# Performance work log

Measured on AMD Instinct MI355X. Metric: run time of the kernel, lower is better.

## Reference

```python
import jax, jax.numpy as jnp
import numpy as np

N_NODES = 50000
N_EDGES = 800000
N_ATOMS = 100
HID = 128
N_LAYERS = 3
OUT_LAYERS = 2
OUT_DIM = 1
N_GRAPHS = 1024
EPS = 1e-12  # F.normalize eps


def setup_inputs() -> dict:
    key = jax.random.key(0)
    ks = jax.random.split(key, 12)
    s = 0.05
    x_ori = jax.random.randint(ks[0], (N_NODES,), 0, N_ATOMS)
    edge_index = jax.random.randint(ks[1], (2, N_EDGES), 0, N_NODES)
    edge_attr = jax.random.normal(ks[2], (N_EDGES, 1), jnp.float32)
    batch_ids = jnp.sort(jax.random.randint(ks[3], (N_NODES,), 0, N_GRAPHS))
    embd_w = jax.random.normal(ks[4], (N_ATOMS, HID), jnp.float32) * s
    gamma_w = jnp.ones((N_LAYERS, N_ATOMS, 1), jnp.float32)  # reset_parameters sets ones
    w_atom_W = jax.random.normal(ks[5], (N_LAYERS, HID, HID), jnp.float32) * s
    w_atom_b = jax.random.normal(ks[6], (N_LAYERS, HID), jnp.float32) * s
    lin_W = jax.random.normal(ks[7], (OUT_LAYERS, HID, HID), jnp.float32) * s
    lin_b = jax.random.normal(ks[8], (OUT_LAYERS, HID), jnp.float32) * s
    wp_W = jax.random.normal(ks[9], (HID, OUT_DIM), jnp.float32) * s
    wp_b = jax.random.normal(ks[10], (OUT_DIM,), jnp.float32) * s
    return dict(x_ori=x_ori, edge_index=edge_index, edge_attr=edge_attr,
                batch_ids=batch_ids, embd_w=embd_w, gamma_w=gamma_w,
                w_atom_W=w_atom_W, w_atom_b=w_atom_b, lin_W=lin_W, lin_b=lin_b,
                wp_W=wp_W, wp_b=wp_b)


def reference(x_ori, edge_index, edge_attr, batch_ids, embd_w, gamma_w,
              w_atom_W, w_atom_b, lin_W, lin_b, wp_W, wp_b):
    src, dst = edge_index[0], edge_index[1]
    x = embd_w[x_ori]  # [N, H]
    for l in range(N_LAYERS):
        h = jax.nn.relu(x @ w_atom_W[l] + w_atom_b[l])            # [N, H]
        gam = jax.nn.sigmoid(gamma_w[l])[x_ori][dst]              # [E, 1]
        ew = jnp.exp(-gam * edge_attr ** 2)                       # [E, 1]
        msg = ew * h[src]                                         # [E, H] gather+weight
        agg = jax.ops.segment_sum(msg, dst, num_segments=N_NODES) # scatter-add
        y = agg + x
        nrm = jnp.maximum(jnp.linalg.norm(y, axis=1, keepdims=True), EPS)
        x = y / nrm                                               # F.normalize(., 2, 1)
    for i in range(OUT_LAYERS):
        x = jax.nn.relu(x @ lin_W[i] + lin_b[i])
    m_x = jax.ops.segment_sum(x, batch_ids, num_segments=N_GRAPHS)  # [G, H]
    props = m_x @ wp_W + wp_b                                      # [G, 1]
    return jnp.squeeze(props, axis=1)                              # [G]
```

## Files before the change

kernel.cpp:

```cpp
#include <hip/hip_runtime.h>
#include <hip/hip_bf16.h>
#include <math.h>

typedef __hip_bfloat16 bf16;
typedef unsigned int uint;
typedef unsigned short ushort;
typedef __attribute__((ext_vector_type(8))) short short8;
typedef __attribute__((ext_vector_type(4))) float f32x4;

#define HID 128
#define NN 50000
#define NE 800000
#define NG 1024
#define NA 100
#define CAP 64

__device__ __forceinline__ uint bf16_rne_hi(float f) {
    uint u = __float_as_uint(f);
    return (u + 0x7fffu + ((u >> 16) & 1u)) & 0xffff0000u;
}
__device__ __forceinline__ uint pack_bf16x2(float lo, float hi) {
    return (bf16_rne_hi(lo) >> 16) | bf16_rne_hi(hi);
}
__device__ __forceinline__ ushort bf16_rne(float f) {
    uint u = __float_as_uint(f);
    return (ushort)((u + 0x7fffu + ((u >> 16) & 1u)) >> 16);
}
__device__ __forceinline__ float load_f(const void* p, int i, int f32) {
    return f32 ? ((const float*)p)[i]
               : __uint_as_float((uint)((const ushort*)p)[i] << 16);
}
__device__ __forceinline__ int detect_f32(const void* emb) {
    const ushort* p = (const ushort*)emb;
    int lane = threadIdx.x & 63;
    float v = __uint_as_float((uint)p[lane * 4] << 16);
    int bad0 = (!(v == v) || fabsf(v) > 1e4f || (v != 0.0f && fabsf(v) < 1e-10f));
    float w = __uint_as_float((uint)p[lane * 4 + 2] << 16);
    int bad1 = (!(w == w) || fabsf(w) > 1e4f || (w != 0.0f && fabsf(w) < 1e-10f));
    int cnt = __popcll(__ballot(bad0)) + __popcll(__ballot(bad1));
    return cnt > 16;
}

#define EMB_BLKS   ((NN * 64) / 256)
#define PACKW_BLKS (5 * 16384 / 256)
#define CVT_CNT    (300 + 384 + 256 + 128 + 1)
#define CVT_BLKS   5
#define INITC_BLKS ((NN + 255) / 256)
#define PREP_B1    EMB_BLKS
#define PREP_B2    (PREP_B1 + PACKW_BLKS)
#define PREP_B3    (PREP_B2 + CVT_BLKS)
#define PREP_B4    (PREP_B3 + INITC_BLKS)
#define PREP_B5    (PREP_B4 + 4)
#define PREP_GRID  (PREP_B5 + 1)

__global__ void prep_k(const int* __restrict__ xo, const void* __restrict__ emb,
                       const void* __restrict__ gamw, const void* __restrict__ wAW,
                       const void* __restrict__ wAb, const void* __restrict__ linW,
                       const void* __restrict__ linb, const void* __restrict__ wpW,
                       const void* __restrict__ wpb,
                       uint* __restrict__ xb, ushort* __restrict__ Wp,
                       float* __restrict__ f_sgam, float* __restrict__ f_wAb,
                       float* __restrict__ f_linb, float* __restrict__ f_wp,
                       float* __restrict__ f_wpb, int* __restrict__ cursor,
                       float* __restrict__ grf, int* __restrict__ flag) {
    int f32 = detect_f32(emb);
    int b = blockIdx.x, t = threadIdx.x;
    if (b < PREP_B1) {
        int g = b * 256 + t;
        int node = g >> 6, c2 = g & 63;
        int base = xo[node] * HID + c2 * 2;
        xb[g] = pack_bf16x2(load_f(emb, base, f32), load_f(emb, base + 1, f32));
    } else if (b < PREP_B2) {
        int t2 = (b - PREP_B1) * 256 + t;
        int i   = t2 & 7;
        int n   = (t2 >> 3) & 15;
        int q   = (t2 >> 7) & 3;
        int j16 = (t2 >> 9) & 7;
        int ks  = (t2 >> 12) & 3;
        int mat = t2 >> 14;
        int k = ks * 32 + q * 8 + i;
        int j = j16 * 16 + n;
        const void* W = (mat < 3) ? wAW : linW;
        int off = ((mat < 3) ? mat : (mat - 3)) * 16384 + k * HID + j;
        Wp[t2] = bf16_rne(load_f(W, off, f32));
    } else if (b < PREP_B3) {
        int idx = (b - PREP_B2) * 256 + t;
        if (idx < 300) {
            float v = load_f(gamw, idx, f32);
            f_sgam[idx] = 1.0f / (1.0f + __expf(-v));
        } else if (idx < 684) {
            f_wAb[idx - 300] = load_f(wAb, idx - 300, f32);
        } else if (idx < 940) {
            f_linb[idx - 684] = load_f(linb, idx - 684, f32);
        } else if (idx < 1068) {
            f_wp[idx - 940] = load_f(wpW, idx - 940, f32);
        } else if (idx < CVT_CNT) {
            f_wpb[0] = load_f(wpb, 0, f32);
        }
    } else if (b < PREP_B4) {
        int n = (b - PREP_B3) * 256 + t;
        if (n < NN) cursor[n] = n * CAP;
    } else if (b < PREP_B5) {
        grf[(b - PREP_B4) * 256 + t] = 0.0f;
    } else {
        if (t == 0) *flag = f32;
    }
}

__device__ __forceinline__ void gemm_core(const uint* __restrict__ xb,
                                          const ushort* __restrict__ Wp,
                                          const float* __restrict__ bias,
                                          int m0, int lane,
                                          f32x4 acc0[8], f32x4 acc1[8]) {
    int ln15 = lane & 15;
    int q    = lane >> 4;
    int mA = min(m0 + ln15, NN - 1);
    int mB = min(m0 + 16 + ln15, NN - 1);
    const short8* A8 = (const short8*)xb;
    const short8* B8 = (const short8*)Wp;
#pragma unroll
    for (int j16 = 0; j16 < 8; ++j16) {
        float bv = bias[j16 * 16 + ln15];
        acc0[j16] = (f32x4){bv, bv, bv, bv};
        acc1[j16] = acc0[j16];
    }
#pragma unroll
    for (int ks = 0; ks < 4; ++ks) {
        short8 a0 = A8[mA * 16 + ks * 4 + q];
        short8 a1 = A8[mB * 16 + ks * 4 + q];
#pragma unroll
        for (int j16 = 0; j16 < 8; ++j16) {
            short8 b = B8[(ks * 8 + j16) * 64 + q * 16 + ln15];
            acc0[j16] = __builtin_amdgcn_mfma_f32_16x16x32_bf16(a0, b, acc0[j16], 0, 0, 0);
            acc1[j16] = __builtin_amdgcn_mfma_f32_16x16x32_bf16(a1, b, acc1[j16], 0, 0, 0);
        }
    }
}

__device__ __forceinline__ void gemm_store(f32x4 acc0[8], f32x4 acc1[8],
                                           int m0, int lane, uint* __restrict__ outb) {
    int ln15 = lane & 15;
    int q    = lane >> 4;
    ushort* ob = (ushort*)outb;
#pragma unroll
    for (int reg = 0; reg < 4; ++reg) {
        int n0 = m0 + q * 4 + reg;
        int n1 = n0 + 16;
#pragma unroll
        for (int j16 = 0; j16 < 8; ++j16) {
            if (n0 < NN)
                ob[(size_t)n0 * HID + j16 * 16 + ln15] = bf16_rne(fmaxf(acc0[j16][reg], 0.0f));
            if (n1 < NN)
                ob[(size_t)n1 * HID + j16 * 16 + ln15] = bf16_rne(fmaxf(acc1[j16][reg], 0.0f));
        }
    }
}

#define GEMM_BLKS ((NN + 127) / 128)
#define SCAT_BLKS (NE / 4 / 256)
__global__ __launch_bounds__(256) void work2_k(const uint* __restrict__ xb,
                                               const ushort* __restrict__ Wp,
                                               const float* __restrict__ bias,
                                               uint* __restrict__ outb,
                                               const int* __restrict__ esrc,
                                               const int* __restrict__ edst,
                                               const void* __restrict__ ea,
                                               const void* __restrict__ emb,
                                               int* __restrict__ cursor,
                                               uint* __restrict__ csr) {
    int b = blockIdx.x;
    if (b < GEMM_BLKS) {
        f32x4 acc0[8], acc1[8];
        int m0 = b * 128 + (threadIdx.x >> 6) * 32;
        gemm_core(xb, Wp, bias, m0, threadIdx.x & 63, acc0, acc1);
        gemm_store(acc0, acc1, m0, threadIdx.x & 63, outb);
    } else {
        int f32 = detect_f32(emb);
        int e0 = ((b - GEMM_BLKS) * 256 + threadIdx.x) * 4;
        int4 s4 = *(const int4*)(esrc + e0);
        int4 d4 = *(const int4*)(edst + e0);
        float a0, a1, a2, a3;
        if (f32) {
            float4 f = *(const float4*)((const float*)ea + e0);
            a0 = f.x; a1 = f.y; a2 = f.z; a3 = f.w;
        } else {
            ushort4 u = *(const ushort4*)((const ushort*)ea + e0);
            a0 = __uint_as_float((uint)u.x << 16);
            a1 = __uint_as_float((uint)u.y << 16);
            a2 = __uint_as_float((uint)u.z << 16);
            a3 = __uint_as_float((uint)u.w << 16);
        }
        int p0 = atomicAdd(&cursor[d4.x], 1);
        int p1 = atomicAdd(&cursor[d4.y], 1);
        int p2 = atomicAdd(&cursor[d4.z], 1);
        int p3 = atomicAdd(&cursor[d4.w], 1);
        if (p0 < d4.x * CAP + CAP) csr[p0] = (uint)(s4.x & 0xffff) | bf16_rne_hi(a0 * a0);
        if (p1 < d4.y * CAP + CAP) csr[p1] = (uint)(s4.y & 0xffff) | bf16_rne_hi(a1 * a1);
        if (p2 < d4.z * CAP + CAP) csr[p2] = (uint)(s4.z & 0xffff) | bf16_rne_hi(a2 * a2);
        if (p3 < d4.w * CAP + CAP) csr[p3] = (uint)(s4.w & 0xffff) | bf16_rne_hi(a3 * a3);
    }
}

__global__ __launch_bounds__(512) void gg_k(const int* __restrict__ cursor,
                                            const uint* __restrict__ csr,
                                            const int* __restrict__ xo,
                                            const float* __restrict__ sgam,
                                            const uint* __restrict__ hb_in,
                                            uint* __restrict__ xb,
                                            const ushort* __restrict__ Wp,
                                            const float* __restrict__ bias,
                                            uint* __restrict__ hb_out) {
    __shared__ uint lds_a[2048];
    int t = threadIdx.x;
    int w = t >> 6, lane = t & 63;
    int n0 = blockIdx.x * 32;

#pragma unroll
    for (int j4 = 0; j4 < 4; ++j4) {
        int j = w * 4 + j4;
        int n = n0 + j;
        if (n < NN) {
            int deg = min(cursor[n] - n * CAP, CAP);
            const uint* cp = csr + n * CAP;
            float g = sgam[xo[n]];
            float ax = 0.0f, ay = 0.0f;
            for (int e = 0; e < deg; e += 8) {
                uint4 c0 = *(const uint4*)(cp + e);
                uint4 c1 = *(const uint4*)(cp + e + 4);
                uint cc[8];
                cc[0] = c0.x; cc[1] = c0.y; cc[2] = c0.z; cc[3] = c0.w;
                cc[4] = c1.x; cc[5] = c1.y; cc[6] = c1.z; cc[7] = c1.w;
#pragma unroll
                for (int i = 1; i < 8; ++i) cc[i] = (e + i < deg) ? cc[i] : cc[0];
                uint v[8];
#pragma unroll
                for (int i = 0; i < 8; ++i) v[i] = hb_in[(cc[i] & 0xffffu) * 64 + lane];
                float we[8];
#pragma unroll
                for (int i = 0; i < 8; ++i) {
                    float x = __expf(-g * __uint_as_float(cc[i] & 0xffff0000u));
                    we[i] = (e + i < deg) ? x : 0.0f;
                }
#pragma unroll
                for (int i = 0; i < 8; ++i) {
                    ax = fmaf(we[i], __uint_as_float(v[i] << 16), ax);
                    ay = fmaf(we[i], __uint_as_float(v[i] & 0xffff0000u), ay);
                }
            }
            uint xv = xb[n * 64 + lane];
            float yx = ax + __uint_as_float(xv << 16);
            float yy = ay + __uint_as_float(xv & 0xffff0000u);
            float ss = yx * yx + yy * yy;
#pragma unroll
            for (int m = 32; m; m >>= 1) ss += __shfl_xor(ss, m);
            float inv = 1.0f / fmaxf(sqrtf(ss), 1e-12f);
            uint o = pack_bf16x2(yx * inv, yy * inv);
            xb[n * 64 + lane] = o;
            int rt = j >> 4, m = j & 15;
            int ks = lane >> 4, q = (lane >> 2) & 3;
            lds_a[(((rt * 4 + ks) * 64) + q * 16 + m) * 4 + (lane & 3)] = o;
        }
    }
    __syncthreads();

    int ln15 = lane & 15, q = lane >> 4;
    const short8* A8 = (const short8*)lds_a;
    const short8* B8 = (const short8*)Wp;
    f32x4 acc[2];
    {
        float bv = bias[w * 16 + ln15];
        acc[0] = (f32x4){bv, bv, bv, bv};
        acc[1] = acc[0];
    }
#pragma unroll
    for (int ks = 0; ks < 4; ++ks) {
        short8 b = B8[(ks * 8 + w) * 64 + q * 16 + ln15];
#pragma unroll
        for (int rt = 0; rt < 2; ++rt) {
            short8 a = A8[(rt * 4 + ks) * 64 + lane];
            acc[rt] = __builtin_amdgcn_mfma_f32_16x16x32_bf16(a, b, acc[rt], 0, 0, 0);
        }
    }
    ushort* ob = (ushort*)hb_out;
#pragma unroll
    for (int rt = 0; rt < 2; ++rt) {
#pragma unroll
        for (int reg = 0; reg < 4; ++reg) {
            int n = n0 + rt * 16 + q * 4 + reg;
            if (n < NN)
                ob[(size_t)n * HID + w * 16 + ln15] = bf16_rne(fmaxf(acc[rt][reg], 0.0f));
        }
    }
}

__global__ __launch_bounds__(256) void gemm5_graph_k(const uint* __restrict__ xb,
                                                     const ushort* __restrict__ Wp,
                                                     const float* __restrict__ bias,
                                                     const float* __restrict__ wp,
                                                     const int* __restrict__ batch,
                                                     float* __restrict__ grf) {
    int lane = threadIdx.x & 63;
    int ln15 = lane & 15;
    int q    = lane >> 4;
    int m0 = blockIdx.x * 128 + (threadIdx.x >> 6) * 32;
    f32x4 acc0[8], acc1[8];
    gemm_core(xb, Wp, bias, m0, lane, acc0, acc1);
    float wpv[8];
#pragma unroll
    for (int j16 = 0; j16 < 8; ++j16) wpv[j16] = wp[j16 * 16 + ln15];
#pragma unroll
    for (int half = 0; half < 2; ++half) {
#pragma unroll
        for (int reg = 0; reg < 4; ++reg) {
            float s = 0.0f;
#pragma unroll
            for (int j16 = 0; j16 < 8; ++j16) {
                float v = half ? acc1[j16][reg] : acc0[j16][reg];
                s = fmaf(fmaxf(v, 0.0f), wpv[j16], s);
            }
#pragma unroll
            for (int m = 1; m < 16; m <<= 1) s += __shfl_xor(s, m);
            int n = m0 + half * 16 + q * 4 + reg;
            if (ln15 == 0 && n < NN) atomicAdd(&grf[batch[n]], s);
        }
    }
}

__global__ void out_k(const float* __restrict__ grf, const float* __restrict__ wpb,
                      void* __restrict__ out, const int* __restrict__ flag) {
    int g = blockIdx.x * 256 + threadIdx.x;
    if (g >= NG) return;
    float r = grf[g] + wpb[0];
    if (*flag) ((float*)out)[g] = r;
    else       ((bf16*)out)[g] = __float2bfloat16(r);
}

extern "C" void kernel_launch(void* const* d_in, const int* in_sizes, int n_in,
                              void* d_out, int out_size, void* d_ws, size_t ws_size,
                              hipStream_t stream) {
    const int*  xo    = (const int*)d_in[0];
    const int*  ei    = (const int*)d_in[1];
    const int*  src   = ei;
    const int*  dst   = ei + NE;
    const void* ea    = d_in[2];
    const int*  batch = (const int*)d_in[3];
    const void* emb   = d_in[4];
    const void* gamw  = d_in[5];
    const void* wAW   = d_in[6];
    const void* wAb   = d_in[7];
    const void* linW  = d_in[8];
    const void* linb  = d_in[9];
    const void* wpW   = d_in[10];
    const void* wpb   = d_in[11];

    uint*  xb     = (uint*)d_ws;
    uint*  hA     = xb + (size_t)NN * 64;
    uint*  hB     = hA + (size_t)NN * 64;
    uint*  csr    = hB + (size_t)NN * 64;
    int*   cursor = (int*)(csr + (size_t)NN * CAP);
    float* grf    = (float*)(cursor + NN);
    float* P      = grf + NG;
    float* f_sgam = P;
    float* f_wAb  = f_sgam + 304;
    float* f_linb = f_wAb + 384;
    float* f_wp   = f_linb + 256;
    float* f_wpb  = f_wp + 128;
    int*   flag   = (int*)(f_wpb + 8);
    ushort* Wp    = (ushort*)(flag + 8);

    prep_k<<<PREP_GRID, 256, 0, stream>>>(xo, emb, gamw, wAW, wAb, linW, linb, wpW, wpb,
                                          xb, Wp, f_sgam, f_wAb, f_linb, f_wp, f_wpb,
                                          cursor, grf, flag);

    work2_k<<<GEMM_BLKS + SCAT_BLKS, 256, 0, stream>>>(xb, Wp, f_wAb, hA,
                                                       src, dst, ea, emb, cursor, csr);

    const int GG_GRID = (NN + 31) / 32;
    gg_k<<<GG_GRID, 512, 0, stream>>>(cursor, csr, xo, f_sgam,       hA, xb,
                                      Wp + 1 * 16384, f_wAb + 128, hB);
    gg_k<<<GG_GRID, 512, 0, stream>>>(cursor, csr, xo, f_sgam + 100, hB, xb,
                                      Wp + 2 * 16384, f_wAb + 256, hA);
    gg_k<<<GG_GRID, 512, 0, stream>>>(cursor, csr, xo, f_sgam + 200, hA, xb,
                                      Wp + 3 * 16384, f_linb,       hB);

    gemm5_graph_k<<<GEMM_BLKS, 256, 0, stream>>>(hB, Wp + 4 * 16384, f_linb + HID,
                                                 f_wp, batch, grf);
    out_k<<<(NG + 255) / 256, 256, 0, stream>>>(grf, f_wpb, d_out, flag);
}
```

Before: 295.5 us.

## Bucket edges by destination before CSR build and fuse final linear into last layer

Edge scattering into per-node CSR slots now happens in two passes. First, edges are binned by destination into 98 buckets of 512 nodes, using block-local histograms and one global atomic per bucket. Then one block per bucket writes the CSR using LDS atomics for degrees, replacing global per-node cursor atomics. The last graph layer kernel is templated to also run the final linear layer and the per-graph readout from LDS, which removes the separate gemm5 kernel and the write and re-read of hB. It adds a memset, and the buckets have a fixed capacity of 10240, so records beyond that are silently dropped if a bucket overflows.

```diff
diff --git a/kernel.cpp b/kernel.cpp
--- a/kernel.cpp
+++ b/kernel.cpp
@@ -14,6 +14,9 @@
 #define NG 1024
 #define NA 100
 #define CAP 64
+
+#define NB   98
+#define RCAP 10240
 
 __device__ __forceinline__ uint bf16_rne_hi(float f) {
     uint u = __float_as_uint(f);
@@ -41,37 +44,94 @@
     return cnt > 16;
 }
 
+#define A_BLKS     196
 #define EMB_BLKS   ((NN * 64) / 256)
 #define PACKW_BLKS (5 * 16384 / 256)
 #define CVT_CNT    (300 + 384 + 256 + 128 + 1)
 #define CVT_BLKS   5
-#define INITC_BLKS ((NN + 255) / 256)
-#define PREP_B1    EMB_BLKS
-#define PREP_B2    (PREP_B1 + PACKW_BLKS)
-#define PREP_B3    (PREP_B2 + CVT_BLKS)
-#define PREP_B4    (PREP_B3 + INITC_BLKS)
-#define PREP_B5    (PREP_B4 + 4)
-#define PREP_GRID  (PREP_B5 + 1)
+#define PR_B1      A_BLKS
+#define PR_B2      (PR_B1 + EMB_BLKS)
+#define PR_B3      (PR_B2 + PACKW_BLKS)
+#define PR_B4      (PR_B3 + CVT_BLKS)
+#define PR_B5      (PR_B4 + 4)
+#define PREP_GRID  (PR_B5 + 1)
 
 __global__ void prep_k(const int* __restrict__ xo, const void* __restrict__ emb,
                        const void* __restrict__ gamw, const void* __restrict__ wAW,
                        const void* __restrict__ wAb, const void* __restrict__ linW,
                        const void* __restrict__ linb, const void* __restrict__ wpW,
                        const void* __restrict__ wpb,
+                       const int* __restrict__ esrc, const int* __restrict__ edst,
+                       const void* __restrict__ ea,
                        uint* __restrict__ xb, ushort* __restrict__ Wp,
                        float* __restrict__ f_sgam, float* __restrict__ f_wAb,
                        float* __restrict__ f_linb, float* __restrict__ f_wp,
-                       float* __restrict__ f_wpb, int* __restrict__ cursor,
+                       float* __restrict__ f_wpb,
+                       uint2* __restrict__ rec, int* __restrict__ bcur,
                        float* __restrict__ grf, int* __restrict__ flag) {
     int f32 = detect_f32(emb);
     int b = blockIdx.x, t = threadIdx.x;
-    if (b < PREP_B1) {
-        int g = b * 256 + t;
+    if (b < PR_B1) {
+        __shared__ int hist[NB];
+        __shared__ int obase[NB];
+        if (t < NB) hist[t] = 0;
+        __syncthreads();
+        int  dv[16];
+        uint rv[16];
+#pragma unroll
+        for (int k = 0; k < 4; ++k) {
+            int e = b * 4096 + k * 1024 + t * 4;
+            if (e + 3 < NE) {
+                int4 s4 = *(const int4*)(esrc + e);
+                int4 d4 = *(const int4*)(edst + e);
+                float a0, a1, a2, a3;
+                if (f32) {
+                    float4 f = *(const float4*)((const float*)ea + e);
+                    a0 = f.x; a1 = f.y; a2 = f.z; a3 = f.w;
+                } else {
+                    ushort4 u = *(const ushort4*)((const ushort*)ea + e);
+                    a0 = __uint_as_float((uint)u.x << 16);
+                    a1 = __uint_as_float((uint)u.y << 16);
+                    a2 = __uint_as_float((uint)u.z << 16);
+                    a3 = __uint_as_float((uint)u.w << 16);
+                }
+                atomicAdd(&hist[d4.x >> 9], 1);
+                atomicAdd(&hist[d4.y >> 9], 1);
+                atomicAdd(&hist[d4.z >> 9], 1);
+                atomicAdd(&hist[d4.w >> 9], 1);
+                dv[k * 4 + 0] = d4.x; rv[k * 4 + 0] = (uint)(s4.x & 0xffff) | ((uint)bf16_rne(a0 * a0) << 16);
+                dv[k * 4 + 1] = d4.y; rv[k * 4 + 1] = (uint)(s4.y & 0xffff) | ((uint)bf16_rne(a1 * a1) << 16);
+                dv[k * 4 + 2] = d4.z; rv[k * 4 + 2] = (uint)(s4.z & 0xffff) | ((uint)bf16_rne(a2 * a2) << 16);
+                dv[k * 4 + 3] = d4.w; rv[k * 4 + 3] = (uint)(s4.w & 0xffff) | ((uint)bf16_rne(a3 * a3) << 16);
+            } else {
+                dv[k * 4 + 0] = dv[k * 4 + 1] = dv[k * 4 + 2] = dv[k * 4 + 3] = -1;
+                rv[k * 4 + 0] = rv[k * 4 + 1] = rv[k * 4 + 2] = rv[k * 4 + 3] = 0;
+            }
+        }
+        __syncthreads();
+        if (t < NB) {
+            int c = hist[t];
+            obase[t] = c ? atomicAdd(&bcur[t], c) : 0;
+            hist[t] = 0;
+        }
+        __syncthreads();
+#pragma unroll
+        for (int k = 0; k < 16; ++k) {
+            int d = dv[k];
+            if (d >= 0) {
+                int bb = d >> 9;
+                int r = atomicAdd(&hist[bb], 1);
+                int idx = obase[bb] + r;
+                if (idx < RCAP) rec[bb * RCAP + idx] = make_uint2(rv[k], (uint)d);
+            }
+        }
+    } else if (b < PR_B2) {
+        int g = (b - PR_B1) * 256 + t;
         int node = g >> 6, c2 = g & 63;
         int base = xo[node] * HID + c2 * 2;
         xb[g] = pack_bf16x2(load_f(emb, base, f32), load_f(emb, base + 1, f32));
-    } else if (b < PREP_B2) {
-        int t2 = (b - PREP_B1) * 256 + t;
+    } else if (b < PR_B3) {
+        int t2 = (b - PR_B2) * 256 + t;
         int i   = t2 & 7;
         int n   = (t2 >> 3) & 15;
         int q   = (t2 >> 7) & 3;
@@ -83,8 +143,8 @@
         const void* W = (mat < 3) ? wAW : linW;
         int off = ((mat < 3) ? mat : (mat - 3)) * 16384 + k * HID + j;
         Wp[t2] = bf16_rne(load_f(W, off, f32));
-    } else if (b < PREP_B3) {
-        int idx = (b - PREP_B2) * 256 + t;
+    } else if (b < PR_B4) {
+        int idx = (b - PR_B3) * 256 + t;
         if (idx < 300) {
             float v = load_f(gamw, idx, f32);
             f_sgam[idx] = 1.0f / (1.0f + __expf(-v));
@@ -97,11 +157,8 @@
         } else if (idx < CVT_CNT) {
             f_wpb[0] = load_f(wpb, 0, f32);
         }
-    } else if (b < PREP_B4) {
-        int n = (b - PREP_B3) * 256 + t;
-        if (n < NN) cursor[n] = n * CAP;
-    } else if (b < PREP_B5) {
-        grf[(b - PREP_B4) * 256 + t] = 0.0f;
+    } else if (b < PR_B5) {
+        grf[(b - PR_B4) * 256 + t] = 0.0f;
     } else {
         if (t == 0) *flag = f32;
     }
@@ -156,52 +213,41 @@
     }
 }
 
-#define GEMM_BLKS ((NN + 127) / 128)
-#define SCAT_BLKS (NE / 4 / 256)
-__global__ __launch_bounds__(256) void work2_k(const uint* __restrict__ xb,
+#define G1_BLKS ((NN + 255) / 256)
+__global__ __launch_bounds__(512) void work2_k(const uint* __restrict__ xb,
                                                const ushort* __restrict__ Wp,
                                                const float* __restrict__ bias,
                                                uint* __restrict__ outb,
-                                               const int* __restrict__ esrc,
-                                               const int* __restrict__ edst,
-                                               const void* __restrict__ ea,
-                                               const void* __restrict__ emb,
-                                               int* __restrict__ cursor,
-                                               uint* __restrict__ csr) {
-    int b = blockIdx.x;
-    if (b < GEMM_BLKS) {
+                                               const uint2* __restrict__ rec,
+                                               const int* __restrict__ bcur,
+                                               uint* __restrict__ csr,
+                                               int* __restrict__ degarr) {
+    int b = blockIdx.x, t = threadIdx.x;
+    if (b < NB) {
+        __shared__ int ldeg[512];
+        ldeg[t] = 0;
+        __syncthreads();
+        int cnt = min(bcur[b], RCAP);
+        int nb0 = b << 9;
+        for (int i = t; i < cnt; i += 512) {
+            uint2 r = rec[b * RCAP + i];
+            int dst = (int)r.y;
+            int p = atomicAdd(&ldeg[dst - nb0], 1);
+            if (p < CAP) csr[dst * CAP + p] = r.x;
+        }
+        __syncthreads();
+        int n = nb0 + t;
+        if (n < NN) degarr[n] = min(ldeg[t], CAP);
+    } else {
         f32x4 acc0[8], acc1[8];
-        int m0 = b * 128 + (threadIdx.x >> 6) * 32;
-        gemm_core(xb, Wp, bias, m0, threadIdx.x & 63, acc0, acc1);
-        gemm_store(acc0, acc1, m0, threadIdx.x & 63, outb);
-    } else {
-        int f32 = detect_f32(emb);
-        int e0 = ((b - GEMM_BLKS) * 256 + threadIdx.x) * 4;
-        int4 s4 = *(const int4*)(esrc + e0);
-        int4 d4 = *(const int4*)(edst + e0);
-        float a0, a1, a2, a3;
-        if (f32) {
-            float4 f = *(const float4*)((const float*)ea + e0);
-            a0 = f.x; a1 = f.y; a2 = f.z; a3 = f.w;
-        } else {
-            ushort4 u = *(const ushort4*)((const ushort*)ea + e0);
-            a0 = __uint_as_float((uint)u.x << 16);
-            a1 = __uint_as_float((uint)u.y << 16);
-            a2 = __uint_as_float((uint)u.z << 16);
-            a3 = __uint_as_float((uint)u.w << 16);
-        }
-        int p0 = atomicAdd(&cursor[d4.x], 1);
-        int p1 = atomicAdd(&cursor[d4.y], 1);
-        int p2 = atomicAdd(&cursor[d4.z], 1);
-        int p3 = atomicAdd(&cursor[d4.w], 1);
-        if (p0 < d4.x * CAP + CAP) csr[p0] = (uint)(s4.x & 0xffff) | bf16_rne_hi(a0 * a0);
-        if (p1 < d4.y * CAP + CAP) csr[p1] = (uint)(s4.y & 0xffff) | bf16_rne_hi(a1 * a1);
-        if (p2 < d4.z * CAP + CAP) csr[p2] = (uint)(s4.z & 0xffff) | bf16_rne_hi(a2 * a2);
-        if (p3 < d4.w * CAP + CAP) csr[p3] = (uint)(s4.w & 0xffff) | bf16_rne_hi(a3 * a3);
-    }
-}
-
-__global__ __launch_bounds__(512) void gg_k(const int* __restrict__ cursor,
+        int m0 = (b - NB) * 256 + (t >> 6) * 32;
+        gemm_core(xb, Wp, bias, m0, t & 63, acc0, acc1);
+        gemm_store(acc0, acc1, m0, t & 63, outb);
+    }
+}
+
+template<int LAST>
+__global__ __launch_bounds__(512) void gg_k(const int* __restrict__ degarr,
                                             const uint* __restrict__ csr,
                                             const int* __restrict__ xo,
                                             const float* __restrict__ sgam,
@@ -209,8 +255,15 @@
                                             uint* __restrict__ xb,
                                             const ushort* __restrict__ Wp,
                                             const float* __restrict__ bias,
-                                            uint* __restrict__ hb_out) {
-    __shared__ uint lds_a[2048];
+                                            uint* __restrict__ hb_out,
+                                            const ushort* __restrict__ Wp2,
+                                            const float* __restrict__ bias2,
+                                            const float* __restrict__ wp,
+                                            const int* __restrict__ batch,
+                                            float* __restrict__ grf) {
+    __shared__ uint  lds_a[2048];
+    __shared__ uint  lds_b[LAST ? 2048 : 1];
+    __shared__ float lds_p[LAST ? 256 : 1];
     int t = threadIdx.x;
     int w = t >> 6, lane = t & 63;
     int n0 = blockIdx.x * 32;
@@ -220,7 +273,7 @@
         int j = w * 4 + j4;
         int n = n0 + j;
         if (n < NN) {
-            int deg = min(cursor[n] - n * CAP, CAP);
+            int deg = degarr[n];
             const uint* cp = csr + n * CAP;
             float g = sgam[xo[n]];
             float ax = 0.0f, ay = 0.0f;
@@ -255,7 +308,7 @@
             for (int m = 32; m; m >>= 1) ss += __shfl_xor(ss, m);
             float inv = 1.0f / fmaxf(sqrtf(ss), 1e-12f);
             uint o = pack_bf16x2(yx * inv, yy * inv);
-            xb[n * 64 + lane] = o;
+            if (!LAST) xb[n * 64 + lane] = o;
             int rt = j >> 4, m = j & 15;
             int ks = lane >> 4, q = (lane >> 2) & 3;
             lds_a[(((rt * 4 + ks) * 64) + q * 16 + m) * 4 + (lane & 3)] = o;
@@ -274,54 +327,73 @@
     }
 #pragma unroll
     for (int ks = 0; ks < 4; ++ks) {
-        short8 b = B8[(ks * 8 + w) * 64 + q * 16 + ln15];
+        short8 b = B8[(ks * 8 + w) * 64 + lane];
 #pragma unroll
         for (int rt = 0; rt < 2; ++rt) {
             short8 a = A8[(rt * 4 + ks) * 64 + lane];
             acc[rt] = __builtin_amdgcn_mfma_f32_16x16x32_bf16(a, b, acc[rt], 0, 0, 0);
         }
     }
-    ushort* ob = (ushort*)hb_out;
-#pragma unroll
-    for (int rt = 0; rt < 2; ++rt) {
-#pragma unroll
-        for (int reg = 0; reg < 4; ++reg) {
-            int n = n0 + rt * 16 + q * 4 + reg;
-            if (n < NN)
-                ob[(size_t)n * HID + w * 16 + ln15] = bf16_rne(fmaxf(acc[rt][reg], 0.0f));
-        }
-    }
-}
-
-__global__ __launch_bounds__(256) void gemm5_graph_k(const uint* __restrict__ xb,
-                                                     const ushort* __restrict__ Wp,
-                                                     const float* __restrict__ bias,
-                                                     const float* __restrict__ wp,
-                                                     const int* __restrict__ batch,
-                                                     float* __restrict__ grf) {
-    int lane = threadIdx.x & 63;
-    int ln15 = lane & 15;
-    int q    = lane >> 4;
-    int m0 = blockIdx.x * 128 + (threadIdx.x >> 6) * 32;
-    f32x4 acc0[8], acc1[8];
-    gemm_core(xb, Wp, bias, m0, lane, acc0, acc1);
-    float wpv[8];
-#pragma unroll
-    for (int j16 = 0; j16 < 8; ++j16) wpv[j16] = wp[j16 * 16 + ln15];
-#pragma unroll
-    for (int half = 0; half < 2; ++half) {
-#pragma unroll
-        for (int reg = 0; reg < 4; ++reg) {
+    if (!LAST) {
+        ushort* ob = (ushort*)hb_out;
+#pragma unroll
+        for (int rt = 0; rt < 2; ++rt) {
+#pragma unroll
+            for (int reg = 0; reg < 4; ++reg) {
+                int n = n0 + rt * 16 + q * 4 + reg;
+                if (n < NN)
+                    ob[(size_t)n * HID + w * 16 + ln15] = bf16_rne(fmaxf(acc[rt][reg], 0.0f));
+            }
+        }
+    } else {
+        ushort* sb = (ushort*)lds_b;
+        int c  = w * 16 + ln15;
+        int c2 = c >> 1, cb = c2 & 3, cq = (c2 >> 2) & 3, cks = c2 >> 4, lohi = c & 1;
+#pragma unroll
+        for (int rt = 0; rt < 2; ++rt) {
+#pragma unroll
+            for (int reg = 0; reg < 4; ++reg) {
+                int m = q * 4 + reg;
+                int uidx = ((rt * 4 + cks) * 64 + cq * 16 + m) * 4 + cb;
+                sb[uidx * 2 + lohi] = bf16_rne(fmaxf(acc[rt][reg], 0.0f));
+            }
+        }
+        __syncthreads();
+        const short8* A8b = (const short8*)lds_b;
+        const short8* B8b = (const short8*)Wp2;
+        f32x4 acc3[2];
+        {
+            float bv = bias2[w * 16 + ln15];
+            acc3[0] = (f32x4){bv, bv, bv, bv};
+            acc3[1] = acc3[0];
+        }
+#pragma unroll
+        for (int ks = 0; ks < 4; ++ks) {
+            short8 bb = B8b[(ks * 8 + w) * 64 + lane];
+#pragma unroll
+            for (int rt = 0; rt < 2; ++rt) {
+                short8 a = A8b[(rt * 4 + ks) * 64 + lane];
+                acc3[rt] = __builtin_amdgcn_mfma_f32_16x16x32_bf16(a, bb, acc3[rt], 0, 0, 0);
+            }
+        }
+        float wv = wp[w * 16 + ln15];
+#pragma unroll
+        for (int rt = 0; rt < 2; ++rt) {
+#pragma unroll
+            for (int reg = 0; reg < 4; ++reg) {
+                float p = fmaxf(acc3[rt][reg], 0.0f) * wv;
+                p += __shfl_xor(p, 1); p += __shfl_xor(p, 2);
+                p += __shfl_xor(p, 4); p += __shfl_xor(p, 8);
+                if (ln15 == 0) lds_p[(rt * 16 + q * 4 + reg) * 8 + w] = p;
+            }
+        }
+        __syncthreads();
+        if (t < 32) {
             float s = 0.0f;
 #pragma unroll
-            for (int j16 = 0; j16 < 8; ++j16) {
-                float v = half ? acc1[j16][reg] : acc0[j16][reg];
-                s = fmaf(fmaxf(v, 0.0f), wpv[j16], s);
-            }
-#pragma unroll
-            for (int m = 1; m < 16; m <<= 1) s += __shfl_xor(s, m);
-            int n = m0 + half * 16 + q * 4 + reg;
-            if (ln15 == 0 && n < NN) atomicAdd(&grf[batch[n]], s);
+            for (int k = 0; k < 8; ++k) s += lds_p[t * 8 + k];
+            int n = n0 + t;
+            if (n < NN) atomicAdd(&grf[batch[n]], s);
         }
     }
 }
@@ -356,9 +428,10 @@
     uint*  xb     = (uint*)d_ws;
     uint*  hA     = xb + (size_t)NN * 64;
     uint*  hB     = hA + (size_t)NN * 64;
+    uint2* rec    = (uint2*)hB;
     uint*  csr    = hB + (size_t)NN * 64;
-    int*   cursor = (int*)(csr + (size_t)NN * CAP);
-    float* grf    = (float*)(cursor + NN);
+    int*   degarr = (int*)(csr + (size_t)NN * CAP);
+    float* grf    = (float*)(degarr + NN);
     float* P      = grf + NG;
     float* f_sgam = P;
     float* f_wAb  = f_sgam + 304;
@@ -367,23 +440,27 @@
     float* f_wpb  = f_wp + 128;
     int*   flag   = (int*)(f_wpb + 8);
     ushort* Wp    = (ushort*)(flag + 8);
+    int*   bcur   = (int*)(Wp + 5 * 16384);
+
+    hipMemsetAsync(bcur, 0, NB * sizeof(int), stream);
 
     prep_k<<<PREP_GRID, 256, 0, stream>>>(xo, emb, gamw, wAW, wAb, linW, linb, wpW, wpb,
+                                          src, dst, ea,
                                           xb, Wp, f_sgam, f_wAb, f_linb, f_wp, f_wpb,
-                                          cursor, grf, flag);
-
-    work2_k<<<GEMM_BLKS + SCAT_BLKS, 256, 0, stream>>>(xb, Wp, f_wAb, hA,
-                                                       src, dst, ea, emb, cursor, csr);
+                                          rec, bcur, grf, flag);
+
+    work2_k<<<NB + G1_BLKS, 512, 0, stream>>>(xb, Wp, f_wAb, hA, rec, bcur, csr, degarr);
 
     const int GG_GRID = (NN + 31) / 32;
-    gg_k<<<GG_GRID, 512, 0, stream>>>(cursor, csr, xo, f_sgam,       hA, xb,
-                                      Wp + 1 * 16384, f_wAb + 128, hB);
-    gg_k<<<GG_GRID, 512, 0, stream>>>(cursor, csr, xo, f_sgam + 100, hB, xb,
-                                      Wp + 2 * 16384, f_wAb + 256, hA);
-    gg_k<<<GG_GRID, 512, 0, stream>>>(cursor, csr, xo, f_sgam + 200, hA, xb,
-                                      Wp + 3 * 16384, f_linb,       hB);
-
-    gemm5_graph_k<<<GEMM_BLKS, 256, 0, stream>>>(hB, Wp + 4 * 16384, f_linb + HID,
-                                                 f_wp, batch, grf);
+    gg_k<0><<<GG_GRID, 512, 0, stream>>>(degarr, csr, xo, f_sgam,       hA, xb,
+                                         Wp + 1 * 16384, f_wAb + 128, hB,
+                                         nullptr, nullptr, nullptr, nullptr, nullptr);
+    gg_k<0><<<GG_GRID, 512, 0, stream>>>(degarr, csr, xo, f_sgam + 100, hB, xb,
+                                         Wp + 2 * 16384, f_wAb + 256, hA,
+                                         nullptr, nullptr, nullptr, nullptr, nullptr);
+    gg_k<1><<<GG_GRID, 512, 0, stream>>>(degarr, csr, xo, f_sgam + 200, hA, xb,
+                                         Wp + 3 * 16384, f_linb,      nullptr,
+                                         Wp + 4 * 16384, f_linb + HID, f_wp, batch, grf);
+
     out_k<<<(NG + 255) / 256, 256, 0, stream>>>(grf, f_wpb, d_out, flag);
 }
```

Result: no change. 295.3 us (-0.1%).
